# Optimization experiments

Hardware: AMD Instinct MI355X
Metric: run time of the kernel (lower is better)

The kernel has to match this reference:

```python
import jax, jax.numpy as jnp
import numpy as np

IN_DIM = 1024
HID = 256
OUT_DIM = 1000
NUM_BINS = 51
BATCH = 2048
N_LEGAL = 200


def setup_inputs() -> dict:
    key = jax.random.key(0)
    ks = jax.random.split(key, 12)
    s = lambda fan_in: 1.0 / np.sqrt(fan_in)
    u = lambda k, shp, b: jax.random.uniform(k, shp, jnp.float32, -b, b)
    return {
        "x": jax.random.normal(ks[0], (BATCH, IN_DIM), jnp.float32),
        # weights stored as [in, out] (math-equivalent to torch Linear)
        "w_in": u(ks[1], (IN_DIM, HID), s(IN_DIM)),
        "b_in": u(ks[2], (HID,), s(IN_DIM)),
        "w_ah": u(ks[3], (HID, HID), s(HID)),
        "b_ah": u(ks[4], (HID,), s(HID)),
        "w_ao": u(ks[5], (HID, OUT_DIM * NUM_BINS), s(HID)),
        "b_ao": u(ks[6], (OUT_DIM * NUM_BINS,), s(HID)),
        "w_vh": u(ks[7], (HID, HID), s(HID)),
        "b_vh": u(ks[8], (HID,), s(HID)),
        "w_vo": u(ks[9], (HID, NUM_BINS), s(HID)),
        "b_vo": u(ks[10], (NUM_BINS,), s(HID)),
        "v_range": jnp.linspace(-10.0, 10.0, NUM_BINS, dtype=jnp.float32),
        "possible_moves": jax.random.randint(ks[11], (BATCH, N_LEGAL), 0, OUT_DIM),
    }


def reference(x, w_in, b_in, w_ah, b_ah, w_ao, b_ao, w_vh, b_vh, w_vo, b_vo,
              v_range, possible_moves):
    B = x.shape[0]
    h = jax.nn.relu(x @ w_in + b_in)                       # [B, 256]
    adv_h = jax.nn.relu(h @ w_ah + b_ah)                   # [B, 256]
    val_h = jax.nn.relu(h @ w_vh + b_vh)                   # [B, 256]
    adv = (adv_h @ w_ao + b_ao).reshape(B, OUT_DIM, NUM_BINS)
    val = (val_h @ w_vo + b_vo).reshape(B, 1, NUM_BINS)
    q = val + adv - adv.mean(axis=1, keepdims=True)        # [B, A, bins]
    p = jnp.maximum(jax.nn.softmax(q, axis=2), 1e-5)       # softmax + clamp(min=1e-5)
    q_vals = jnp.sum(p * v_range, axis=2)                  # [B, A]
    # LegalSoftmax: per-row scatter of 1.0 at legal indices, vectorized
    mask = jnp.zeros((B, OUT_DIM), x.dtype).at[
        jnp.arange(B)[:, None], possible_moves].set(1.0)
    filtered = q_vals * mask
    # faithful to torch: any exact-zero entry (masked OR coincidental) -> -inf
    return jnp.where(filtered == 0, -jnp.inf, filtered)
```

## Files before the change

### kernel.cpp

```cpp
#include <hip/hip_runtime.h>
#include <cstdint>
#include <cstddef>

#define NB      2048
#define INDIM   1024
#define HID     256
#define NA      1000
#define BINS    51
#define NLEG    200
#define NPAIR   (NB*NLEG)
#define NBLK    256
#define PPB     (NPAIR/NBLK)
#define KEXT    320

#define NEG_SENTINEL (-1.0e30f)

typedef float    f32x4  __attribute__((ext_vector_type(4)));
typedef __bf16   bf16x8 __attribute__((ext_vector_type(8)));
typedef unsigned short us8 __attribute__((ext_vector_type(8)));

__device__ __forceinline__ unsigned short f2bf(float f) {
  union { float f; unsigned u; } v; v.f = f;
  return (unsigned short)((v.u + 0x7FFFu + ((v.u >> 16) & 1u)) >> 16);
}
__device__ __forceinline__ float bf2f(unsigned short h) {
  union { unsigned u; float f; } v; v.u = ((unsigned)h) << 16;
  return v.f;
}
__device__ __forceinline__ bf16x8 as_bf(us8 v) { return __builtin_bit_cast(bf16x8, v); }
__device__ __forceinline__ int imin(int a, int b) { return a < b ? a : b; }

__global__ __launch_bounds__(256) void k_phase1(
    const float* __restrict__ w_ao, unsigned short* __restrict__ wp,
    float* __restrict__ wmean_acc,
    const float* __restrict__ w_in, const float* __restrict__ w_ah,
    const float* __restrict__ w_vh,
    unsigned short* __restrict__ w_inT, unsigned short* __restrict__ w_ahT,
    unsigned short* __restrict__ w_vhT,
    float* __restrict__ out, const int* __restrict__ pm,
    int* __restrict__ hist) {
  __shared__ __align__(16) char smem[26240];
  int b = blockIdx.x, tid = threadIdx.x;
  if (b < 1000) {
    unsigned short (*st)[410] = (unsigned short(*)[410])smem;
    int s = b & 7, a0 = (b >> 3) * 8;
    for (int i = tid; i < 32 * 408; i += 256) {
      int r = i / 408, cix = i - r * 408;
      st[r][cix] = f2bf(w_ao[(size_t)(s * 32 + r) * (NA * BINS) + a0 * BINS + cix]);
    }
    __syncthreads();
    for (int i = tid; i < 32 * 51; i += 256) {
      int r = i / 51, j = i - r * 51;
      float s8 = 0.f;
#pragma unroll
      for (int aL = 0; aL < 8; aL++) s8 += bf2f(st[r][aL * BINS + j]);
      atomicAdd(&wmean_acc[(size_t)(s * 32 + r) * BINS + j], s8);
    }
    int t = (tid >> 6) & 3, l = tid & 63;
    int col = t * 16 + (l & 15), kg = l >> 4;
    for (int aL = 0; aL < 8; aL++) {
      unsigned short vals[8];
#pragma unroll
      for (int j = 0; j < 8; j++)
        vals[j] = (col < BINS) ? st[kg * 8 + j][aL * BINS + col] : (unsigned short)0;
      size_t fg = ((size_t)(a0 + aL) * 8 + s) * 4 + t;
      *(us8*)(wp + fg * 512 + (size_t)l * 8) = *(const us8*)vals;
    }
  } else if (b < 1884) {
    int bb = b - 1000;
    if (bb < 384) {
      float (*tile)[33] = (float(*)[33])smem;
      const float* w; unsigned short* wT; int K, N, kt, nt;
      if (bb < 256)      { w = w_in; wT = w_inT; K = INDIM; N = HID; kt = bb & 31;        nt = bb >> 5; }
      else if (bb < 320) { w = w_ah; wT = w_ahT; K = HID;   N = HID; kt = (bb - 256) & 7; nt = (bb - 256) >> 3; }
      else               { w = w_vh; wT = w_vhT; K = HID;   N = HID; kt = (bb - 320) & 7; nt = (bb - 320) >> 3; }
      int k0 = kt * 32, n0 = nt * 32;
      int cr = tid >> 5, cc = tid & 31;
#pragma unroll
      for (int it = 0; it < 4; it++)
        tile[cr + it * 8][cc] = w[(size_t)(k0 + cr + it * 8) * N + n0 + cc];
      __syncthreads();
#pragma unroll
      for (int it = 0; it < 4; it++)
        wT[(size_t)(n0 + cr + it * 8) * K + k0 + cc] = f2bf(tile[cc][cr + it * 8]);
    } else {
      int base = (bb - 384) * 1024 + tid;
      float4 v = {NEG_SENTINEL, NEG_SENTINEL, NEG_SENTINEL, NEG_SENTINEL};
#pragma unroll
      for (int it = 0; it < 4; it++) ((float4*)out)[base + it * 256] = v;
    }
  } else {
    int* lh = (int*)smem;
    int blk = b - 1884;
    for (int i = tid; i < NA; i += 256) lh[i] = 0;
    __syncthreads();
    int base = blk * PPB;
    for (int i = tid; i < PPB; i += 256) atomicAdd(&lh[pm[base + i]], 1);
    __syncthreads();
    for (int a = tid; a < NA; a += 256) hist[a * NBLK + blk] = lh[a];
  }
}

__global__ __launch_bounds__(256) void k_phase2(
    int* __restrict__ hist, int* __restrict__ cnt,
    const float* __restrict__ w_vo, const float* __restrict__ wmean_acc,
    const float* __restrict__ b_vo, const float* __restrict__ b_ao,
    unsigned short* __restrict__ Wc, float* __restrict__ bias_c,
    const float* __restrict__ x, const unsigned short* __restrict__ w_inT,
    const float* __restrict__ b_in, unsigned short* __restrict__ h_bf) {
  int b = blockIdx.x, tid = threadIdx.x;
  if (b < 1000) {
    __shared__ int s[256];
    int a = b, t = tid;
    int v = hist[a * NBLK + t];
    s[t] = v;
    __syncthreads();
    for (int d = 1; d < 256; d <<= 1) {
      int u = (t >= d) ? s[t - d] : 0;
      __syncthreads();
      s[t] += u;
      __syncthreads();
    }
    hist[a * NBLK + t] = s[t] - v;
    if (t == 255) cnt[a] = s[255];
  } else if (b < 1064) {
    __shared__ float s[256];
    int n = b - 1000, t = tid;
    for (int k = t; k < 512; k += 256) {
      float v = 0.f;
      if (n < BINS)
        v = (k < 256) ? w_vo[(size_t)k * BINS + n]
                      : (-0.001f * wmean_acc[(size_t)(k - 256) * BINS + n]);
      Wc[(size_t)n * 512 + k] = f2bf(v);
    }
    float acc = 0.f;
    if (n < BINS)
      for (int a = t; a < NA; a += 256) acc += b_ao[(size_t)a * BINS + n];
    s[t] = acc;
    __syncthreads();
    for (int d = 128; d > 0; d >>= 1) { if (t < d) s[t] += s[t + d]; __syncthreads(); }
    if (t == 0) bias_c[n] = (n < BINS) ? (b_vo[n] - 0.001f * s[0]) : 0.f;
  } else {
    int w = tid >> 6, l = tid & 63, la = l & 15, g = l >> 4;
    int idx = (b - 1064) * 4 + w;
    int m0 = (idx & 127) * 16, n0 = (idx >> 7) * 16;
    f32x4 acc = {0.f, 0.f, 0.f, 0.f};
    const us8* Bp = (const us8*)(w_inT + (size_t)(n0 + la) * INDIM) + g;
    const float* Ar = x + (size_t)(m0 + la) * INDIM + g * 8;
    for (int s = 0; s < INDIM; s += 32) {
      float4 f0 = *(const float4*)(Ar + s);
      float4 f1 = *(const float4*)(Ar + s + 4);
      us8 u;
      u[0] = f2bf(f0.x); u[1] = f2bf(f0.y); u[2] = f2bf(f0.z); u[3] = f2bf(f0.w);
      u[4] = f2bf(f1.x); u[5] = f2bf(f1.y); u[6] = f2bf(f1.z); u[7] = f2bf(f1.w);
      acc = __builtin_amdgcn_mfma_f32_16x16x32_bf16(as_bf(u), as_bf(Bp[s >> 3]),
                                                    acc, 0, 0, 0);
    }
    float bb = b_in[n0 + la];
#pragma unroll
    for (int r = 0; r < 4; r++) {
      float v = fmaxf(acc[r] + bb, 0.f);
      h_bf[(size_t)(m0 + g * 4 + r) * HID + n0 + la] = f2bf(v);
    }
  }
}

__global__ __launch_bounds__(256) void k_phase3(
    const int* __restrict__ cnt, int* __restrict__ off,
    const unsigned short* __restrict__ h,
    const unsigned short* __restrict__ wA, const float* __restrict__ bA,
    unsigned short* __restrict__ oA,
    const unsigned short* __restrict__ wV, const float* __restrict__ bV,
    unsigned short* __restrict__ oV) {
  int b = blockIdx.x, tid = threadIdx.x;
  if (b == 1024) {
    __shared__ int s[256];
    int t = tid, i0 = 4 * t;
    int v0 = (i0     < NA) ? cnt[i0]     : 0;
    int v1 = (i0 + 1 < NA) ? cnt[i0 + 1] : 0;
    int v2 = (i0 + 2 < NA) ? cnt[i0 + 2] : 0;
    int v3 = (i0 + 3 < NA) ? cnt[i0 + 3] : 0;
    int sum = v0 + v1 + v2 + v3;
    s[t] = sum;
    __syncthreads();
    for (int d = 1; d < 256; d <<= 1) {
      int u = (t >= d) ? s[t - d] : 0;
      __syncthreads();
      s[t] += u;
      __syncthreads();
    }
    int excl = s[t] - sum;
    if (i0     < NA) off[i0]     = excl;
    if (i0 + 1 < NA) off[i0 + 1] = excl + v0;
    if (i0 + 2 < NA) off[i0 + 2] = excl + v0 + v1;
    if (i0 + 3 < NA) off[i0 + 3] = excl + v0 + v1 + v2;
  } else {
    int w = tid >> 6, l = tid & 63, la = l & 15, g = l >> 4;
    int idx = b * 4 + w;
    int m0 = (idx & 127) * 16;
    int ny = idx >> 7;
    int second = ny >> 4;
    int n0 = (ny & 15) * 16;
    const unsigned short* BT = second ? wV : wA;
    const float* bias = second ? bV : bA;
    unsigned short* ob = second ? oV : oA;
    int ldo = second ? HID : KEXT;
    f32x4 acc = {0.f, 0.f, 0.f, 0.f};
    const us8* Bp = (const us8*)(BT + (size_t)(n0 + la) * HID) + g;
    const us8* Ap = (const us8*)(h + (size_t)(m0 + la) * HID) + g;
#pragma unroll
    for (int s = 0; s < 8; s++)
      acc = __builtin_amdgcn_mfma_f32_16x16x32_bf16(as_bf(Ap[s * 4]), as_bf(Bp[s * 4]),
                                                    acc, 0, 0, 0);
    float bb = bias[n0 + la];
#pragma unroll
    for (int r = 0; r < 4; r++) {
      float v = fmaxf(acc[r] + bb, 0.f);
      ob[(size_t)(m0 + g * 4 + r) * ldo + n0 + la] = f2bf(v);
    }
  }
}

__global__ __launch_bounds__(256) void k_phase4(
    const int* __restrict__ pm, const int* __restrict__ off,
    const int* __restrict__ hist, int* __restrict__ rows,
    const unsigned short* __restrict__ valh, const unsigned short* __restrict__ Aext,
    const unsigned short* __restrict__ Wc, const float* __restrict__ bias_c,
    unsigned short* __restrict__ outc) {
  int b = blockIdx.x, tid = threadIdx.x;
  if (b < 256) {
    __shared__ int lc[NA];
    __shared__ int lbase[NA];
    int blk = b, t = tid;
    for (int i = t; i < NA; i += 256) {
      lc[i] = 0;
      lbase[i] = off[i] + hist[i * NBLK + blk];
    }
    __syncthreads();
    int base = blk * PPB;
    for (int i = t; i < PPB; i += 256) {
      int a = pm[base + i];
      int r = atomicAdd(&lc[a], 1);
      rows[lbase[a] + r] = (base + i) / NLEG;
    }
  } else {
    int w = tid >> 6, l = tid & 63, la = l & 15, g = l >> 4;
    int idx = (b - 256) * 4 + w;
    int m0 = (idx & 127) * 16, n0 = (idx >> 7) * 16;
    f32x4 acc = {0.f, 0.f, 0.f, 0.f};
    const us8* Bp  = (const us8*)(Wc + (size_t)(n0 + la) * 512) + g;
    const us8* Ap1 = (const us8*)(valh + (size_t)(m0 + la) * HID) + g;
    const us8* Ap2 = (const us8*)(Aext + (size_t)(m0 + la) * KEXT) + g;
#pragma unroll
    for (int s = 0; s < 8; s++)
      acc = __builtin_amdgcn_mfma_f32_16x16x32_bf16(as_bf(Ap1[s * 4]), as_bf(Bp[s * 4]),
                                                    acc, 0, 0, 0);
#pragma unroll
    for (int s = 0; s < 8; s++)
      acc = __builtin_amdgcn_mfma_f32_16x16x32_bf16(as_bf(Ap2[s * 4]), as_bf(Bp[(8 + s) * 4]),
                                                    acc, 0, 0, 0);
    float bb = bias_c[n0 + la];
#pragma unroll
    for (int r = 0; r < 4; r++)
      outc[(size_t)(m0 + g * 4 + r) * KEXT + n0 + la] = f2bf(acc[r] + bb);
  }
}

__global__ __launch_bounds__(256) void k_main_mfma(
    const unsigned short* __restrict__ Aext,
    const unsigned short* __restrict__ wp,
    const float* __restrict__ b_ao,
    const float* __restrict__ v_range,
    const int* __restrict__ cnt, const int* __restrict__ off,
    const int* __restrict__ rows,
    float* __restrict__ out) {
  __shared__ us8 sB[2048];
  int bx = blockIdx.x;
  int a = (bx & 7) * 125 + (bx >> 3);
  int count = cnt[a];
  int ntiles = (count + 15) >> 4;
  if ((int)(blockIdx.y * 4) >= ntiles) return;
  int tid = threadIdx.x;
  const us8* wpa = (const us8*)wp + (size_t)a * 2048;
  for (int i = tid; i < 2048; i += 256) sB[i] = wpa[i];
  __syncthreads();

  int w = tid >> 6, l = tid & 63, la = l & 15, g = l >> 4;
  int base = off[a];
  float vr[4], bao[4];
#pragma unroll
  for (int t = 0; t < 4; t++) {
    int bin = t * 16 + la;
    bool vb = bin < BINS;
    vr[t]  = vb ? v_range[bin] : 0.f;
    bao[t] = vb ? b_ao[(size_t)a * BINS + bin] : 0.f;
  }

  for (int tile = blockIdx.y * 4 + w; tile < ntiles; tile += 8) {
    int m16 = tile * 16;
    int rA = rows[base + imin(m16 + la, count - 1)];
    const us8* Ap = (const us8*)(Aext + (size_t)rA * KEXT) + g;
    f32x4 acc[4];
#pragma unroll
    for (int t = 0; t < 4; t++) acc[t] = (f32x4){0.f, 0.f, 0.f, 0.f};
#pragma unroll
    for (int s = 0; s < 8; s++) {
      bf16x8 af = as_bf(Ap[s * 4]);
#pragma unroll
      for (int t = 0; t < 4; t++)
        acc[t] = __builtin_amdgcn_mfma_f32_16x16x32_bf16(
            af, as_bf(sB[(s * 4 + t) * 64 + l]), acc[t], 0, 0, 0);
    }
    {
      us8 a8 = Ap[32], a9 = Ap[36];
#pragma unroll
      for (int t = 0; t < 4; t++) {
        int colg = t * 16 + la;
        us8 u0, u1;
#pragma unroll
        for (int j = 0; j < 8; j++) {
          u0[j] = (g * 8 + j == colg)      ? (unsigned short)0x3F80 : (unsigned short)0;
          u1[j] = (g * 8 + j + 32 == colg) ? (unsigned short)0x3F80 : (unsigned short)0;
        }
        acc[t] = __builtin_amdgcn_mfma_f32_16x16x32_bf16(as_bf(a8), as_bf(u0), acc[t], 0, 0, 0);
        acc[t] = __builtin_amdgcn_mfma_f32_16x16x32_bf16(as_bf(a9), as_bf(u1), acc[t], 0, 0, 0);
      }
    }
#pragma unroll
    for (int r = 0; r < 4; r++) {
      int gi = m16 + g * 4 + r;
      bool vrow = gi < count;
      int b = __shfl(rA, g * 4 + r, 16);
      float e[4];
      float S = 0.f;
#pragma unroll
      for (int t = 0; t < 4; t++) {
        int bin = t * 16 + la;
        float v = (bin < BINS) ? (acc[t][r] + bao[t]) : -1.0e30f;
        e[t] = __expf(v);
        S += e[t];
      }
#pragma unroll
      for (int i = 1; i < 16; i <<= 1) S += __shfl_xor(S, i);
      float inv = 1.f / S;
      float qv = 0.f;
#pragma unroll
      for (int t = 0; t < 4; t++) {
        int bin = t * 16 + la;
        if (bin < BINS) qv = fmaf(fmaxf(e[t] * inv, 1e-5f), vr[t], qv);
      }
#pragma unroll
      for (int i = 1; i < 16; i <<= 1) qv += __shfl_xor(qv, i);
      if (vrow && la == 0)
        out[(size_t)b * NA + a] = (qv == 0.f) ? NEG_SENTINEL : qv;
    }
  }
}

extern "C" void kernel_launch(void* const* d_in, const int* in_sizes, int n_in,
                              void* d_out, int out_size, void* d_ws, size_t ws_size,
                              hipStream_t stream) {
  (void)in_sizes; (void)n_in; (void)out_size; (void)ws_size;
  const float* x     = (const float*)d_in[0];
  const float* w_in  = (const float*)d_in[1];
  const float* b_in  = (const float*)d_in[2];
  const float* w_ah  = (const float*)d_in[3];
  const float* b_ah  = (const float*)d_in[4];
  const float* w_ao  = (const float*)d_in[5];
  const float* b_ao  = (const float*)d_in[6];
  const float* w_vh  = (const float*)d_in[7];
  const float* b_vh  = (const float*)d_in[8];
  const float* w_vo  = (const float*)d_in[9];
  const float* b_vo  = (const float*)d_in[10];
  const float* v_rng = (const float*)d_in[11];
  const int*   pm    = (const int*)d_in[12];
  float* out = (float*)d_out;

  char* p = (char*)d_ws;
  unsigned short* wp      = (unsigned short*)p; p += (size_t)NA * 8 * 4 * 512 * 2;
  unsigned short* h_bf    = (unsigned short*)p; p += (size_t)NB * HID * 2;
  unsigned short* valh_bf = (unsigned short*)p; p += (size_t)NB * HID * 2;
  unsigned short* Aext    = (unsigned short*)p; p += (size_t)NB * KEXT * 2;
  unsigned short* w_inT   = (unsigned short*)p; p += (size_t)HID * INDIM * 2;
  unsigned short* w_ahT   = (unsigned short*)p; p += (size_t)HID * HID * 2;
  unsigned short* w_vhT   = (unsigned short*)p; p += (size_t)HID * HID * 2;
  unsigned short* Wc      = (unsigned short*)p; p += (size_t)64 * 512 * 2;
  float* bias_c = (float*)p; p += 64 * 4;
  float* wmean  = (float*)p; p += 13056 * 4;
  int* cnt  = (int*)p; p += NA * 4;
  int* off  = (int*)p; p += NA * 4;
  int* hist = (int*)p; p += (size_t)NA * NBLK * 4;
  int* rows = (int*)p; p += (size_t)NPAIR * 4 + 256;

  hipMemsetAsync(wmean, 0, 13056 * sizeof(float), stream);

  k_phase1<<<2140, 256, 0, stream>>>(w_ao, wp, wmean, w_in, w_ah, w_vh,
                                     w_inT, w_ahT, w_vhT, out, pm, hist);
  k_phase2<<<1576, 256, 0, stream>>>(hist, cnt, w_vo, wmean, b_vo, b_ao,
                                     Wc, bias_c, x, w_inT, b_in, h_bf);
  k_phase3<<<1025, 256, 0, stream>>>(cnt, off, h_bf, w_ahT, b_ah, Aext,
                                     w_vhT, b_vh, valh_bf);
  k_phase4<<<384, 256, 0, stream>>>(pm, off, hist, rows, valh_bf, Aext,
                                    Wc, bias_c, Aext + 256);
  k_main_mfma<<<dim3(1000, 2), 256, 0, stream>>>(Aext, wp, b_ao, v_rng,
                                                 cnt, off, rows, out);
}
```

Measured before the change: 240.3 us.

## Quantize advantage-head weights and activations to FP8 for the main MFMA

```diff
diff --git a/kernel.cpp b/kernel.cpp
--- a/kernel.cpp
+++ b/kernel.cpp
@@ -11,13 +11,13 @@
 #define NPAIR   (NB*NLEG)
 #define NBLK    256
 #define PPB     (NPAIR/NBLK)
-#define KEXT    320
 
 #define NEG_SENTINEL (-1.0e30f)
 
 typedef float    f32x4  __attribute__((ext_vector_type(4)));
 typedef __bf16   bf16x8 __attribute__((ext_vector_type(8)));
 typedef unsigned short us8 __attribute__((ext_vector_type(8)));
+typedef unsigned long long u64x2 __attribute__((ext_vector_type(2)));
 
 __device__ __forceinline__ unsigned short f2bf(float f) {
   union { float f; unsigned u; } v; v.f = f;
@@ -30,8 +30,22 @@
 __device__ __forceinline__ bf16x8 as_bf(us8 v) { return __builtin_bit_cast(bf16x8, v); }
 __device__ __forceinline__ int imin(int a, int b) { return a < b ? a : b; }
 
+__device__ __forceinline__ unsigned f2fp8x4(float a, float b, float c, float d) {
+  int v = 0;
+  v = __builtin_amdgcn_cvt_pk_fp8_f32(a, b, v, false);
+  v = __builtin_amdgcn_cvt_pk_fp8_f32(c, d, v, true);
+  return (unsigned)v;
+}
+__device__ __forceinline__ unsigned char f2fp8(float f) {
+  int v = __builtin_amdgcn_cvt_pk_fp8_f32(f, 0.f, 0, false);
+  return (unsigned char)(v & 0xff);
+}
+__device__ __forceinline__ float fp82f(unsigned char u) {
+  return __builtin_amdgcn_cvt_f32_fp8((int)u, 0);
+}
+
 __global__ __launch_bounds__(256) void k_phase1(
-    const float* __restrict__ w_ao, unsigned short* __restrict__ wp,
+    const float* __restrict__ w_ao, unsigned char* __restrict__ wp8,
     float* __restrict__ wmean_acc,
     const float* __restrict__ w_in, const float* __restrict__ w_ah,
     const float* __restrict__ w_vh,
@@ -42,29 +56,37 @@
   __shared__ __align__(16) char smem[26240];
   int b = blockIdx.x, tid = threadIdx.x;
   if (b < 1000) {
-    unsigned short (*st)[410] = (unsigned short(*)[410])smem;
+    unsigned char* st = (unsigned char*)smem;
     int s = b & 7, a0 = (b >> 3) * 8;
-    for (int i = tid; i < 32 * 408; i += 256) {
-      int r = i / 408, cix = i - r * 408;
-      st[r][cix] = f2bf(w_ao[(size_t)(s * 32 + r) * (NA * BINS) + a0 * BINS + cix]);
+    const float* wbase = w_ao + (size_t)(s * 32) * (NA * BINS) + a0 * BINS;
+    for (int i = tid; i < 32 * 102; i += 256) {
+      int r = i / 102, c4 = i - r * 102;
+      float4 f = *(const float4*)(wbase + (size_t)r * (NA * BINS) + c4 * 4);
+      *(unsigned*)(st + r * 420 + c4 * 4) =
+          f2fp8x4(f.x * 16.f, f.y * 16.f, f.z * 16.f, f.w * 16.f);
     }
     __syncthreads();
     for (int i = tid; i < 32 * 51; i += 256) {
       int r = i / 51, j = i - r * 51;
       float s8 = 0.f;
 #pragma unroll
-      for (int aL = 0; aL < 8; aL++) s8 += bf2f(st[r][aL * BINS + j]);
+      for (int aL = 0; aL < 8; aL++) s8 += fp82f(st[r * 420 + aL * 51 + j]);
       atomicAdd(&wmean_acc[(size_t)(s * 32 + r) * BINS + j], s8);
     }
-    int t = (tid >> 6) & 3, l = tid & 63;
-    int col = t * 16 + (l & 15), kg = l >> 4;
+    int t4 = (tid >> 6) & 3, l = tid & 63;
+    int col = t4 * 16 + (l & 15), kg = l >> 4;
     for (int aL = 0; aL < 8; aL++) {
-      unsigned short vals[8];
-#pragma unroll
-      for (int j = 0; j < 8; j++)
-        vals[j] = (col < BINS) ? st[kg * 8 + j][aL * BINS + col] : (unsigned short)0;
-      size_t fg = ((size_t)(a0 + aL) * 8 + s) * 4 + t;
-      *(us8*)(wp + fg * 512 + (size_t)l * 8) = *(const us8*)vals;
+      unsigned lo = 0, hi = 0;
+      if (col < BINS) {
+        const unsigned char* p0 = st + (kg * 8) * 420 + aL * 51 + col;
+        lo = (unsigned)p0[0] | ((unsigned)p0[420] << 8) |
+             ((unsigned)p0[840] << 16) | ((unsigned)p0[1260] << 24);
+        hi = (unsigned)p0[1680] | ((unsigned)p0[2100] << 8) |
+             ((unsigned)p0[2520] << 16) | ((unsigned)p0[2940] << 24);
+      }
+      size_t fg = ((size_t)(a0 + aL) * 8 + s) * 4 + t4;
+      uint2 v; v.x = lo; v.y = hi;
+      *(uint2*)(wp8 + fg * 512 + (size_t)l * 8) = v;
     }
   } else if (b < 1884) {
     int bb = b - 1000;
@@ -130,7 +152,7 @@
       float v = 0.f;
       if (n < BINS)
         v = (k < 256) ? w_vo[(size_t)k * BINS + n]
-                      : (-0.001f * wmean_acc[(size_t)(k - 256) * BINS + n]);
+                      : (-(0.001f / 16.f) * wmean_acc[(size_t)(k - 256) * BINS + n]);
       Wc[(size_t)n * 512 + k] = f2bf(v);
     }
     float acc = 0.f;
@@ -169,7 +191,7 @@
     const int* __restrict__ cnt, int* __restrict__ off,
     const unsigned short* __restrict__ h,
     const unsigned short* __restrict__ wA, const float* __restrict__ bA,
-    unsigned short* __restrict__ oA,
+    unsigned char* __restrict__ Aext8, unsigned short* __restrict__ advh_bf,
     const unsigned short* __restrict__ wV, const float* __restrict__ bV,
     unsigned short* __restrict__ oV) {
   int b = blockIdx.x, tid = threadIdx.x;
@@ -203,8 +225,6 @@
     int n0 = (ny & 15) * 16;
     const unsigned short* BT = second ? wV : wA;
     const float* bias = second ? bV : bA;
-    unsigned short* ob = second ? oV : oA;
-    int ldo = second ? HID : KEXT;
     f32x4 acc = {0.f, 0.f, 0.f, 0.f};
     const us8* Bp = (const us8*)(BT + (size_t)(n0 + la) * HID) + g;
     const us8* Ap = (const us8*)(h + (size_t)(m0 + la) * HID) + g;
@@ -216,7 +236,13 @@
 #pragma unroll
     for (int r = 0; r < 4; r++) {
       float v = fmaxf(acc[r] + bb, 0.f);
-      ob[(size_t)(m0 + g * 4 + r) * ldo + n0 + la] = f2bf(v);
+      size_t o = (size_t)(m0 + g * 4 + r) * HID + n0 + la;
+      if (second) {
+        oV[o] = f2bf(v);
+      } else {
+        advh_bf[o] = f2bf(v);
+        Aext8[o] = f2fp8(v);
+      }
     }
   }
 }
@@ -224,9 +250,9 @@
 __global__ __launch_bounds__(256) void k_phase4(
     const int* __restrict__ pm, const int* __restrict__ off,
     const int* __restrict__ hist, int* __restrict__ rows,
-    const unsigned short* __restrict__ valh, const unsigned short* __restrict__ Aext,
+    const unsigned short* __restrict__ valh, const unsigned short* __restrict__ advh,
     const unsigned short* __restrict__ Wc, const float* __restrict__ bias_c,
-    unsigned short* __restrict__ outc) {
+    unsigned short* __restrict__ cbuf) {
   int b = blockIdx.x, tid = threadIdx.x;
   if (b < 256) {
     __shared__ int lc[NA];
@@ -250,7 +276,7 @@
     f32x4 acc = {0.f, 0.f, 0.f, 0.f};
     const us8* Bp  = (const us8*)(Wc + (size_t)(n0 + la) * 512) + g;
     const us8* Ap1 = (const us8*)(valh + (size_t)(m0 + la) * HID) + g;
-    const us8* Ap2 = (const us8*)(Aext + (size_t)(m0 + la) * KEXT) + g;
+    const us8* Ap2 = (const us8*)(advh + (size_t)(m0 + la) * HID) + g;
 #pragma unroll
     for (int s = 0; s < 8; s++)
       acc = __builtin_amdgcn_mfma_f32_16x16x32_bf16(as_bf(Ap1[s * 4]), as_bf(Bp[s * 4]),
@@ -262,27 +288,28 @@
     float bb = bias_c[n0 + la];
 #pragma unroll
     for (int r = 0; r < 4; r++)
-      outc[(size_t)(m0 + g * 4 + r) * KEXT + n0 + la] = f2bf(acc[r] + bb);
+      cbuf[(size_t)(m0 + g * 4 + r) * 64 + n0 + la] = f2bf(acc[r] + bb);
   }
 }
 
 __global__ __launch_bounds__(256) void k_main_mfma(
-    const unsigned short* __restrict__ Aext,
-    const unsigned short* __restrict__ wp,
+    const unsigned char* __restrict__ Aext8,
+    const unsigned short* __restrict__ cbuf,
+    const unsigned char* __restrict__ wp8,
     const float* __restrict__ b_ao,
     const float* __restrict__ v_range,
     const int* __restrict__ cnt, const int* __restrict__ off,
     const int* __restrict__ rows,
     float* __restrict__ out) {
-  __shared__ us8 sB[2048];
+  __shared__ __align__(16) long long sB8[2048];
   int bx = blockIdx.x;
   int a = (bx & 7) * 125 + (bx >> 3);
   int count = cnt[a];
   int ntiles = (count + 15) >> 4;
   if ((int)(blockIdx.y * 4) >= ntiles) return;
   int tid = threadIdx.x;
-  const us8* wpa = (const us8*)wp + (size_t)a * 2048;
-  for (int i = tid; i < 2048; i += 256) sB[i] = wpa[i];
+  const u64x2* wpa = (const u64x2*)(wp8 + (size_t)a * 16384);
+  for (int i = tid; i < 1024; i += 256) ((u64x2*)sB8)[i] = wpa[i];
   __syncthreads();
 
   int w = tid >> 6, l = tid & 63, la = l & 15, g = l >> 4;
@@ -299,31 +326,32 @@
   for (int tile = blockIdx.y * 4 + w; tile < ntiles; tile += 8) {
     int m16 = tile * 16;
     int rA = rows[base + imin(m16 + la, count - 1)];
-    const us8* Ap = (const us8*)(Aext + (size_t)rA * KEXT) + g;
+    const long long* Ap = (const long long*)(Aext8 + (size_t)rA * HID) + g;
+    const us8* Cp = (const us8*)(cbuf + (size_t)rA * 64) + g;
     f32x4 acc[4];
 #pragma unroll
     for (int t = 0; t < 4; t++) acc[t] = (f32x4){0.f, 0.f, 0.f, 0.f};
 #pragma unroll
     for (int s = 0; s < 8; s++) {
-      bf16x8 af = as_bf(Ap[s * 4]);
+      long long a8 = Ap[s * 4];
 #pragma unroll
       for (int t = 0; t < 4; t++)
-        acc[t] = __builtin_amdgcn_mfma_f32_16x16x32_bf16(
-            af, as_bf(sB[(s * 4 + t) * 64 + l]), acc[t], 0, 0, 0);
+        acc[t] = __builtin_amdgcn_mfma_f32_16x16x32_fp8_fp8(
+            a8, sB8[(s * 4 + t) * 64 + l], acc[t], 0, 0, 0);
     }
     {
-      us8 a8 = Ap[32], a9 = Ap[36];
+      us8 c0 = Cp[0], c1 = Cp[4];
 #pragma unroll
       for (int t = 0; t < 4; t++) {
         int colg = t * 16 + la;
         us8 u0, u1;
 #pragma unroll
         for (int j = 0; j < 8; j++) {
-          u0[j] = (g * 8 + j == colg)      ? (unsigned short)0x3F80 : (unsigned short)0;
-          u1[j] = (g * 8 + j + 32 == colg) ? (unsigned short)0x3F80 : (unsigned short)0;
+          u0[j] = (g * 8 + j == colg)      ? (unsigned short)0x4180 : (unsigned short)0;
+          u1[j] = (g * 8 + j + 32 == colg) ? (unsigned short)0x4180 : (unsigned short)0;
         }
-        acc[t] = __builtin_amdgcn_mfma_f32_16x16x32_bf16(as_bf(a8), as_bf(u0), acc[t], 0, 0, 0);
-        acc[t] = __builtin_amdgcn_mfma_f32_16x16x32_bf16(as_bf(a9), as_bf(u1), acc[t], 0, 0, 0);
+        acc[t] = __builtin_amdgcn_mfma_f32_16x16x32_bf16(as_bf(c0), as_bf(u0), acc[t], 0, 0, 0);
+        acc[t] = __builtin_amdgcn_mfma_f32_16x16x32_bf16(as_bf(c1), as_bf(u1), acc[t], 0, 0, 0);
       }
     }
 #pragma unroll
@@ -336,7 +364,7 @@
 #pragma unroll
       for (int t = 0; t < 4; t++) {
         int bin = t * 16 + la;
-        float v = (bin < BINS) ? (acc[t][r] + bao[t]) : -1.0e30f;
+        float v = (bin < BINS) ? (acc[t][r] * 0.0625f + bao[t]) : -1.0e30f;
         e[t] = __expf(v);
         S += e[t];
       }
@@ -377,10 +405,12 @@
   float* out = (float*)d_out;
 
   char* p = (char*)d_ws;
-  unsigned short* wp      = (unsigned short*)p; p += (size_t)NA * 8 * 4 * 512 * 2;
+  unsigned char*  wp8     = (unsigned char*)p;  p += (size_t)NA * 32 * 512;
+  unsigned char*  Aext8   = (unsigned char*)p;  p += (size_t)NB * HID;
+  unsigned short* cbuf    = (unsigned short*)p; p += (size_t)NB * 64 * 2;
   unsigned short* h_bf    = (unsigned short*)p; p += (size_t)NB * HID * 2;
+  unsigned short* advh_bf = (unsigned short*)p; p += (size_t)NB * HID * 2;
   unsigned short* valh_bf = (unsigned short*)p; p += (size_t)NB * HID * 2;
-  unsigned short* Aext    = (unsigned short*)p; p += (size_t)NB * KEXT * 2;
   unsigned short* w_inT   = (unsigned short*)p; p += (size_t)HID * INDIM * 2;
   unsigned short* w_ahT   = (unsigned short*)p; p += (size_t)HID * HID * 2;
   unsigned short* w_vhT   = (unsigned short*)p; p += (size_t)HID * HID * 2;
@@ -394,14 +424,14 @@
 
   hipMemsetAsync(wmean, 0, 13056 * sizeof(float), stream);
 
-  k_phase1<<<2140, 256, 0, stream>>>(w_ao, wp, wmean, w_in, w_ah, w_vh,
+  k_phase1<<<2140, 256, 0, stream>>>(w_ao, wp8, wmean, w_in, w_ah, w_vh,
                                      w_inT, w_ahT, w_vhT, out, pm, hist);
   k_phase2<<<1576, 256, 0, stream>>>(hist, cnt, w_vo, wmean, b_vo, b_ao,
                                      Wc, bias_c, x, w_inT, b_in, h_bf);
-  k_phase3<<<1025, 256, 0, stream>>>(cnt, off, h_bf, w_ahT, b_ah, Aext,
-                                     w_vhT, b_vh, valh_bf);
-  k_phase4<<<384, 256, 0, stream>>>(pm, off, hist, rows, valh_bf, Aext,
-                                    Wc, bias_c, Aext + 256);
-  k_main_mfma<<<dim3(1000, 2), 256, 0, stream>>>(Aext, wp, b_ao, v_rng,
+  k_phase3<<<1025, 256, 0, stream>>>(cnt, off, h_bf, w_ahT, b_ah, Aext8,
+                                     advh_bf, w_vhT, b_vh, valh_bf);
+  k_phase4<<<384, 256, 0, stream>>>(pm, off, hist, rows, valh_bf, advh_bf,
+                                    Wc, bias_c, cbuf);
+  k_main_mfma<<<dim3(1000, 2), 256, 0, stream>>>(Aext8, cbuf, wp8, b_ao, v_rng,
                                                  cnt, off, rows, out);
 }
```

Result: faster. 220.9 us (-8.1%).
